# Kernel optimization log

Hardware: AMD Instinct MI355X
Metric: run time of the kernel (lower is better)

## Reference

```python
import jax, jax.numpy as jnp
import numpy as np

L = 2        # n_layers
F = 128      # in_features == out_features (GRUCell + highway constraint)
O = 128
N = 1024     # nodes
B = 8        # batch
D = 3        # edge directions (weight.size(0))


def setup_inputs() -> dict:
    key = jax.random.key(0)
    ks = jax.random.split(key, 10)
    s = 1.0 / np.sqrt(F)
    u = lambda k, shp: jax.random.uniform(k, shp, jnp.float32, minval=-s, maxval=s)
    return {
        "inputs": jax.random.normal(ks[0], (N, B, F), jnp.float32),
        "adj": jax.random.uniform(ks[1], (D, B, N, N), jnp.float32),
        "W": u(ks[2], (L, D, F, O)),            # GCN weight per layer/direction
        "Bc": u(ks[3], (L, D, O)),              # GCN bias
        "Wh": u(ks[4], (L, F, O)),              # highway weight
        "Bh": u(ks[5], (L, O)),                 # highway bias
        "Wih": u(ks[6], (L, 3 * O, O)),         # GRUCell input weights
        "Whh": u(ks[7], (L, 3 * O, O)),         # GRUCell hidden weights
        "bih": u(ks[8], (L, 3 * O)),
        "bhh": u(ks[9], (L, 3 * O)),
    }


def _gru(x, h, wih, whh, bih, bhh):
    # torch.nn.GRUCell semantics; x,h: [..., O]
    gi = x @ wih.T + bih
    gh = h @ whh.T + bhh
    i_r, i_z, i_n = jnp.split(gi, 3, axis=-1)
    h_r, h_z, h_n = jnp.split(gh, 3, axis=-1)
    r = jax.nn.sigmoid(i_r + h_r)
    z = jax.nn.sigmoid(i_z + h_z)
    n = jnp.tanh(i_n + r * h_n)
    return (1.0 - z) * n + z * h


def reference(inputs, adj, W, Bc, Wh, Bh, Wih, Whh, bih, bhh):
    x = inputs  # [N, B, F]; dropout layers are identity at eval
    for l in range(L):
        # support per direction: [D, B, N, O]
        support = jnp.einsum('nbf,dfo->dbno', x, W[l]) + Bc[l][:, None, None, :]
        # adjacency-weighted aggregation: adj[d,b] @ support[d,b]
        agg = jnp.einsum('dbmn,dbno->dbmo', adj, support)
        # GRU update with hidden = current features, per direction, summed over d
        h = jnp.broadcast_to(jnp.transpose(x, (1, 0, 2))[None], agg.shape)
        hnew = _gru(agg, h, Wih[l], Whh[l], bih[l], bhh[l])
        out = jnp.transpose(jnp.sum(hnew, axis=0), (1, 0, 2))  # [N, B, O]
        out = jax.nn.relu(out)  # activation='relu'
        # highway gate (highway='relu')
        t = jax.nn.relu(jnp.einsum('nbf,fo->nbo', x, Wh[l]) + Bh[l])
        x = out * t + x * (1.0 - t)
    return x
```

## Files before the change

kernel.cpp:

```cpp
#include <hip/hip_runtime.h>
#include <math.h>

#define N_NODES 1024
#define BATCH   8
#define FEAT    128
#define NDIR    3
#define NB      (N_NODES*BATCH)
#define G3      384

typedef __bf16 bf16_t;
using bf16x8 = __attribute__((ext_vector_type(8))) __bf16;
using bf16x4 = __attribute__((ext_vector_type(4))) __bf16;
using f32x4  = __attribute__((ext_vector_type(4))) float;

#define GLOAD_LDS16(g, l) \
    __builtin_amdgcn_global_load_lds((const __attribute__((address_space(1))) void*)(g), \
                                     (__attribute__((address_space(3))) void*)(l), 16, 0, 0)

template<int R>
__device__ __forceinline__ void stage_swz(const bf16_t* __restrict__ src, int stride,
                                          int k0, bf16_t* lds, int w, int lane)
{
    #pragma unroll
    for (int q = 0; q < R/32; ++q) {
        int rbase = w*(R/4) + q*8;
        int row = rbase + (lane >> 3);
        int seg = (lane & 7) ^ (row & 7);
        GLOAD_LDS16(src + (size_t)row*stride + k0 + seg*8,
                    (char*)lds + (size_t)rbase*128);
    }
}

__device__ __forceinline__ void stageA_f32(const float* __restrict__ src, int k0,
                                           bf16_t* lds, int w, int lane)
{
    #pragma unroll
    for (int q = 0; q < 2; ++q) {
        int rbase = w*16 + q*8;
        int row = rbase + (lane >> 3);
        int s   = lane & 7;
        int seg = s ^ (row & 7);
        const float* g = src + (size_t)row*1024 + k0 + seg*8;
        float4 v0 = *reinterpret_cast<const float4*>(g);
        float4 v1 = *reinterpret_cast<const float4*>(g + 4);
        bf16x8 pk;
        pk[0]=(bf16_t)(v0.x-0.5f); pk[1]=(bf16_t)(v0.y-0.5f);
        pk[2]=(bf16_t)(v0.z-0.5f); pk[3]=(bf16_t)(v0.w-0.5f);
        pk[4]=(bf16_t)(v1.x-0.5f); pk[5]=(bf16_t)(v1.y-0.5f);
        pk[6]=(bf16_t)(v1.z-0.5f); pk[7]=(bf16_t)(v1.w-0.5f);
        *reinterpret_cast<bf16x8*>(&lds[row*64 + s*8]) = pk;
    }
}

template<int MI, int NJ>
__device__ __forceinline__ void mfma_swz(const bf16_t* As, const bf16_t* Bs,
                                         f32x4 (&acc)[MI][NJ], int wr, int wc, int lane)
{
    #pragma unroll
    for (int ks = 0; ks < 64; ks += 32) {
        int bslot = ks/8 + (lane >> 4);
        int sx = bslot ^ (lane & 7);
        bf16x8 af[MI], bfv[NJ];
        #pragma unroll
        for (int i = 0; i < MI; ++i) {
            int row = wr*MI*16 + i*16 + (lane & 15);
            af[i] = *reinterpret_cast<const bf16x8*>(&As[row*64 + sx*8]);
        }
        #pragma unroll
        for (int j = 0; j < NJ; ++j) {
            int row = wc*NJ*16 + j*16 + (lane & 15);
            bfv[j] = *reinterpret_cast<const bf16x8*>(&Bs[row*64 + sx*8]);
        }
        #pragma unroll
        for (int i = 0; i < MI; ++i) {
            #pragma unroll
            for (int j = 0; j < NJ; ++j)
                acc[i][j] = __builtin_amdgcn_mfma_f32_16x16x32_bf16(af[i], bfv[j], acc[i][j], 0, 0, 0);
        }
    }
}

__device__ __forceinline__ float fast_sigmoid(float x)
{
    float t = __builtin_amdgcn_exp2f(-1.442695041f * x);
    return __builtin_amdgcn_rcpf(1.0f + t);
}
__device__ __forceinline__ float fast_tanh(float x)
{
    float ax = fabsf(x);
    float t = __builtin_amdgcn_exp2f(-2.885390082f * ax);
    float r = (1.0f - t) * __builtin_amdgcn_rcpf(1.0f + t);
    return copysignf(r, x);
}

__global__ __launch_bounds__(128) void k_wprep(
    const float* __restrict__ W, const float* __restrict__ Wh,
    const float* __restrict__ Whh, const float* __restrict__ Wih,
    bf16_t* __restrict__ wsup,
    bf16_t* __restrict__ wihc)
{
    int m = blockIdx.x, l = blockIdx.y, k = threadIdx.x;
    float w;
    bf16_t* dst;
    bool patB = false;
    if (m < 384) {
        int d = m >> 7, o = m & 127;
        w = W[((size_t)(l*3 + d)*128 + k)*128 + o];
        dst = wsup + ((size_t)l*896 + m)*384;
    } else if (m < 512) {
        int o = m - 384;
        w = Wh[((size_t)l*128 + k)*128 + o];
        dst = wsup + ((size_t)l*896 + m)*384;
    } else if (m < 896) {
        int c = m - 512;
        w = Whh[((size_t)l*384 + c)*128 + k];
        dst = wsup + ((size_t)l*896 + m)*384;
    } else {
        int c = m - 896;
        w = Wih[((size_t)l*384 + c)*128 + k];
        dst = wihc + ((size_t)l*384 + c)*384;
        patB = true;
    }
    bf16_t hi = (bf16_t)w;
    bf16_t lo = (bf16_t)(w - (float)hi);
    if (patB) { dst[k] = hi; dst[128 + k] = hi; dst[256 + k] = lo; }
    else      { dst[k] = hi; dst[128 + k] = lo; dst[256 + k] = hi; }
}

__global__ __launch_bounds__(256) void k_xcat(
    const float* __restrict__ X, bf16_t* __restrict__ xcat,
    float* __restrict__ colsum2)
{
    int idx = blockIdx.x * 256 + threadIdx.x;
    if (idx < 2*3072) colsum2[idx] = 0.0f;
    int k = idx & 127, r = idx >> 7;
    int n = r >> 3, b = r & 7;
    float v = X[idx];
    bf16_t hi = (bf16_t)v;
    bf16_t lo = (bf16_t)(v - (float)hi);
    bf16_t* dst = xcat + ((size_t)(b*1024 + n))*384 + k;
    dst[0] = hi; dst[128] = hi; dst[256] = lo;
}

__global__ __launch_bounds__(256, 2) void k_sup2(
    const bf16_t* __restrict__ Wcat,
    const bf16_t* __restrict__ xcat,
    const float* __restrict__ Bcl,
    const float* __restrict__ Bhl,
    const float* __restrict__ bhhl,
    bf16_t* __restrict__ supt,
    float* __restrict__ tbuf,
    bf16_t* __restrict__ ghb,
    float* __restrict__ colsum)
{
    __shared__ bf16_t As[2][128*64];
    __shared__ bf16_t Bs[2][128*64];
    const int t = threadIdx.x, lane = t & 63, w = t >> 6;
    const int wr = w >> 1, wc = w & 1;
    const int n0 = blockIdx.x * 128;
    const int m0 = blockIdx.y * 128;
    const int b  = blockIdx.z;
    const bf16_t* Arow = Wcat + (size_t)m0 * 384;
    const bf16_t* Brow = xcat + ((size_t)b * 1024 + n0) * 384;

    f32x4 acc[4][4] = {};
    stage_swz<128>(Arow, 384, 0, As[0], w, lane);
    stage_swz<128>(Brow, 384, 0, Bs[0], w, lane);
    __syncthreads();
    #pragma unroll
    for (int kt = 0; kt < 6; ++kt) {
        if (kt + 1 < 6) {
            stage_swz<128>(Arow, 384, (kt+1)*64, As[(kt+1)&1], w, lane);
            stage_swz<128>(Brow, 384, (kt+1)*64, Bs[(kt+1)&1], w, lane);
        }
        mfma_swz<4,4>(As[kt&1], Bs[kt&1], acc, wr, wc, lane);
        __syncthreads();
    }
    #pragma unroll
    for (int i = 0; i < 4; ++i) {
        int mb = m0 + wr*64 + i*16 + ((lane >> 4) * 4);
        if (mb < 384) {
            #pragma unroll
            for (int rg = 0; rg < 4; ++rg) {
                int m = mb + rg;
                int d = m >> 7, o = m & 127;
                float bv = Bcl[d*128 + o];
                float psum = 0.0f;
                #pragma unroll
                for (int j = 0; j < 4; ++j) {
                    int n = n0 + wc*64 + j*16 + (lane & 15);
                    bf16_t sv = (bf16_t)(acc[i][j][rg] + bv);
                    supt[((size_t)((d*8 + b)*128 + o))*1024 + n] = sv;
                    psum += (float)sv;
                }
                psum += __shfl_xor(psum, 1, 64);
                psum += __shfl_xor(psum, 2, 64);
                psum += __shfl_xor(psum, 4, 64);
                psum += __shfl_xor(psum, 8, 64);
                if ((lane & 15) == 0)
                    atomicAdd(&colsum[(d*8 + b)*128 + o], psum);
            }
        } else if (mb < 512) {
            #pragma unroll
            for (int j = 0; j < 4; ++j) {
                int n = n0 + wc*64 + j*16 + (lane & 15);
                #pragma unroll
                for (int rg = 0; rg < 4; ++rg) {
                    int o = mb + rg - 384;
                    tbuf[((size_t)(b*128 + o))*1024 + n] =
                        fmaxf(acc[i][j][rg] + Bhl[o], 0.0f);
                }
            }
        } else {
            #pragma unroll
            for (int j = 0; j < 4; ++j) {
                int n = n0 + wc*64 + j*16 + (lane & 15);
                int c = mb - 512;
                bf16x4 pk;
                #pragma unroll
                for (int rg = 0; rg < 4; ++rg)
                    pk[rg] = (bf16_t)(acc[i][j][rg] + bhhl[c + rg]);
                *reinterpret_cast<bf16x4*>(&ghb[((size_t)(b*1024 + n))*384 + c]) = pk;
            }
        }
    }
}

__global__ __launch_bounds__(256, 3) void k_agg(
    const float* __restrict__ adjf,
    const bf16_t* __restrict__ supt,
    const float* __restrict__ colsum,
    bf16_t* __restrict__ aggcat)
{
    __shared__ bf16_t As[2][64*64];
    __shared__ bf16_t Bs[2][128*64];
    const int t = threadIdx.x, lane = t & 63, w = t >> 6;
    const int wr = w >> 1, wc = w & 1;
    const int m0 = blockIdx.x * 64;
    const int z  = blockIdx.y;
    const float*  Af = adjf + (size_t)z * 1024 * 1024 + (size_t)m0 * 1024;
    const bf16_t* Brow = supt + (size_t)z * 128 * 1024;

    f32x4 acc[2][4] = {};
    stageA_f32(Af, 0, As[0], w, lane);
    stage_swz<128>(Brow, 1024, 0, Bs[0], w, lane);
    __syncthreads();
    #pragma unroll
    for (int kt = 0; kt < 16; ++kt) {
        if (kt + 1 < 16) {
            stageA_f32(Af, (kt+1)*64, As[(kt+1)&1], w, lane);
            stage_swz<128>(Brow, 1024, (kt+1)*64, Bs[(kt+1)&1], w, lane);
        }
        mfma_swz<2,4>(As[kt&1], Bs[kt&1], acc, wr, wc, lane);
        __syncthreads();
    }
    #pragma unroll
    for (int i = 0; i < 2; ++i) {
        #pragma unroll
        for (int rg = 0; rg < 4; ++rg) {
            size_t m = (size_t)z*1024 + m0 + wr*32 + i*16 + ((lane >> 4) * 4) + rg;
            bf16_t* row = aggcat + m*384;
            #pragma unroll
            for (int j = 0; j < 4; ++j) {
                int o = wc*64 + j*16 + (lane & 15);
                float v = acc[i][j][rg] + 0.5f * colsum[z*128 + o];
                bf16_t hi = (bf16_t)v;
                bf16_t lo = (bf16_t)(v - (float)hi);
                row[o] = hi; row[128 + o] = lo; row[256 + o] = hi;
            }
        }
    }
}

__global__ __launch_bounds__(256, 2) void k_gi(
    const bf16_t* __restrict__ A,
    const bf16_t* __restrict__ B,
    const float*  __restrict__ bias,
    bf16_t* __restrict__ girz,
    float* __restrict__ gin)
{
    __shared__ bf16_t As[2][128*64];
    __shared__ bf16_t Bs[2][128*64];
    const int t = threadIdx.x, lane = t & 63, w = t >> 6;
    const int wr = w >> 1, wc = w & 1;
    const int m0 = blockIdx.x * 128;
    const int c0 = blockIdx.y * 128;
    const bf16_t* Arow = A + (size_t)m0 * 384;
    const bf16_t* Brow = B + (size_t)c0 * 384;

    f32x4 acc[4][4] = {};
    stage_swz<128>(Arow, 384, 0, As[0], w, lane);
    stage_swz<128>(Brow, 384, 0, Bs[0], w, lane);
    __syncthreads();
    #pragma unroll
    for (int kt = 0; kt < 6; ++kt) {
        if (kt + 1 < 6) {
            stage_swz<128>(Arow, 384, (kt+1)*64, As[(kt+1)&1], w, lane);
            stage_swz<128>(Brow, 384, (kt+1)*64, Bs[(kt+1)&1], w, lane);
        }
        mfma_swz<4,4>(As[kt&1], Bs[kt&1], acc, wr, wc, lane);
        __syncthreads();
    }
    #pragma unroll
    for (int j = 0; j < 4; ++j) {
        int c = c0 + wc*64 + j*16 + (lane & 15);
        float bv = bias[c];
        #pragma unroll
        for (int i = 0; i < 4; ++i) {
            #pragma unroll
            for (int rg = 0; rg < 4; ++rg) {
                int m = m0 + wr*64 + i*16 + ((lane >> 4) * 4) + rg;
                float v = acc[i][j][rg] + bv;
                if (c < 256) girz[(size_t)m*256 + c] = (bf16_t)v;
                else         gin[(size_t)m*128 + (c - 256)] = v;
            }
        }
    }
}

__global__ __launch_bounds__(256) void k_gates(
    const bf16_t* __restrict__ girz, const float* __restrict__ gin,
    const bf16_t* __restrict__ ghb,
    bf16_t* xcat,
    const float* __restrict__ tbuf,
    float* __restrict__ Xout, int write_xcat)
{
    __shared__ float ts[128*17];
    const int b = blockIdx.y, n0 = blockIdx.x * 16;
    const int tid = threadIdx.x;
    {
        int o = tid >> 1, nh = (tid & 1) * 8;
        const float* src = tbuf + ((size_t)(b*128 + o))*1024 + n0 + nh;
        float4 v0 = *reinterpret_cast<const float4*>(src);
        float4 v1 = *reinterpret_cast<const float4*>(src + 4);
        float* dst = &ts[o*17 + nh];
        dst[0]=v0.x; dst[1]=v0.y; dst[2]=v0.z; dst[3]=v0.w;
        dst[4]=v1.x; dst[5]=v1.y; dst[6]=v1.z; dst[7]=v1.w;
    }
    __syncthreads();
    #pragma unroll
    for (int p = 0; p < 8; ++p) {
        int e = p*256 + tid;
        int nn = e >> 7, o = e & 127;
        int n = n0 + nn;
        size_t rb = (size_t)(b*1024 + n);
        bf16_t* xr = xcat + rb*384;
        float h = (float)xr[o] + (float)xr[256 + o];
        const bf16_t* ghr = ghb + rb*G3;
        float g_r = (float)ghr[o], g_z = (float)ghr[128+o], g_n = (float)ghr[256+o];
        float acc = 0.0f;
        #pragma unroll
        for (int d = 0; d < 3; ++d) {
            size_t rr = (size_t)((d*8 + b)*1024 + n);
            float i_r = (float)girz[rr*256 + o];
            float i_z = (float)girz[rr*256 + 128 + o];
            float i_n = gin[rr*128 + o];
            float rg = fast_sigmoid(i_r + g_r);
            float zg = fast_sigmoid(i_z + g_z);
            float ng = fast_tanh(i_n + rg * g_n);
            acc += (1.0f - zg) * ng + zg * h;
        }
        float outv = fmaxf(acc, 0.0f);
        float tg = ts[o*17 + nn];
        float res = outv * tg + h * (1.0f - tg);
        if (Xout) Xout[(size_t)(n*8 + b)*128 + o] = res;
        if (write_xcat) {
            bf16_t hi = (bf16_t)res;
            bf16_t lo = (bf16_t)(res - (float)hi);
            xr[o] = hi; xr[128 + o] = hi; xr[256 + o] = lo;
        }
    }
}

extern "C" void kernel_launch(void* const* d_in, const int* in_sizes, int n_in,
                              void* d_out, int out_size, void* d_ws, size_t ws_size,
                              hipStream_t stream) {
    const float* inputs = (const float*)d_in[0];
    const float* adj    = (const float*)d_in[1];
    const float* W      = (const float*)d_in[2];
    const float* Bc     = (const float*)d_in[3];
    const float* Wh     = (const float*)d_in[4];
    const float* Bh     = (const float*)d_in[5];
    const float* Wih    = (const float*)d_in[6];
    const float* Whh    = (const float*)d_in[7];
    const float* bih    = (const float*)d_in[8];
    const float* bhh    = (const float*)d_in[9];

    char* ws = (char*)d_ws;
    float*  tbuf   = (float*)ws;   ws += (size_t)8*128*1024*4;
    bf16_t* xcat   = (bf16_t*)ws;  ws += (size_t)8*1024*384*2;
    bf16_t* ghb    = (bf16_t*)ws;  ws += (size_t)NB*G3*2;
    bf16_t* supt   = (bf16_t*)ws;  ws += (size_t)24*128*1024*2;
    bf16_t* aggcat = (bf16_t*)ws;  ws += (size_t)3*NB*384*2;
    bf16_t* girz   = (bf16_t*)ws;  ws += (size_t)3*NB*256*2;
    float*  gin    = (float*)ws;   ws += (size_t)3*NB*128*4;
    float*  colsum2= (float*)ws;   ws += (size_t)2*24*128*4;
    bf16_t* wsup   = (bf16_t*)ws;  ws += (size_t)2*896*384*2;
    bf16_t* wihc   = (bf16_t*)ws;

    k_wprep<<<dim3(1280, 2), dim3(128), 0, stream>>>(W, Wh, Whh, Wih, wsup, wihc);
    k_xcat<<<dim3(4096), dim3(256), 0, stream>>>(inputs, xcat, colsum2);

    for (int l = 0; l < 2; ++l) {
        float* colsum = colsum2 + l*3072;
        k_sup2<<<dim3(8, 7, 8), dim3(256), 0, stream>>>(
            wsup + (size_t)l*896*384, xcat, Bc + l*3*128, Bh + l*128, bhh + l*G3,
            supt, tbuf, ghb, colsum);
        k_agg<<<dim3(16, 24), dim3(256), 0, stream>>>(adj, supt, colsum, aggcat);
        k_gi<<<dim3(192, 3), dim3(256), 0, stream>>>(
            aggcat, wihc + (size_t)l*384*384, bih + l*G3, girz, gin);
        k_gates<<<dim3(64, 8), dim3(256), 0, stream>>>(
            girz, gin, ghb, xcat, tbuf,
            (l == 1) ? (float*)d_out : (float*)nullptr, (l == 0) ? 1 : 0);
    }
}
```

Baseline: 316.2 us.

## Fuse adjacency aggregation with GRU input-gate GEMM via LDS-resident tile

Merges k_agg and k_gi into one kernel. The aggregated 64x128 tile, split into bf16 hi/lo parts, now stays in shared memory and is multiplied directly by the Wih weights, which stream through a reused LDS pool. This removes the aggcat global round-trip and one kernel launch. In exchange, each block recomputes the GEMM against the full Wih matrix for only 64 rows, occupancy drops from 3 to 2 blocks per CU, and the 24x16=384-block grid is small.

```diff
diff --git a/kernel.cpp b/kernel.cpp
--- a/kernel.cpp
+++ b/kernel.cpp
@@ -226,93 +226,118 @@
     }
 }
 
-__global__ __launch_bounds__(256, 3) void k_agg(
+__device__ __forceinline__ int aggls_off(int row, int k)
+{
+    return row*256 + (((k >> 3) ^ (row & 15)) << 3) + (k & 7);
+}
+
+__global__ __launch_bounds__(256, 2) void k_aggi(
     const float* __restrict__ adjf,
     const bf16_t* __restrict__ supt,
     const float* __restrict__ colsum,
-    bf16_t* __restrict__ aggcat)
-{
-    __shared__ bf16_t As[2][64*64];
-    __shared__ bf16_t Bs[2][128*64];
+    const bf16_t* __restrict__ wihcL,
+    const float* __restrict__ biasL,
+    bf16_t* __restrict__ girz,
+    float* __restrict__ gin)
+{
+    __shared__ char pool[49152];
+    __shared__ bf16_t aggls[64*256];
+    bf16_t* As  = (bf16_t*)pool;
+    bf16_t* Bs  = (bf16_t*)(pool + 16384);
+    bf16_t* BsG = (bf16_t*)pool;
+
     const int t = threadIdx.x, lane = t & 63, w = t >> 6;
     const int wr = w >> 1, wc = w & 1;
     const int m0 = blockIdx.x * 64;
     const int z  = blockIdx.y;
-    const float*  Af = adjf + (size_t)z * 1024 * 1024 + (size_t)m0 * 1024;
+    const float*  Af   = adjf + (size_t)z * 1024 * 1024 + (size_t)m0 * 1024;
     const bf16_t* Brow = supt + (size_t)z * 128 * 1024;
 
     f32x4 acc[2][4] = {};
-    stageA_f32(Af, 0, As[0], w, lane);
-    stage_swz<128>(Brow, 1024, 0, Bs[0], w, lane);
+    stageA_f32(Af, 0, As, w, lane);
+    stage_swz<128>(Brow, 1024, 0, Bs, w, lane);
     __syncthreads();
     #pragma unroll
     for (int kt = 0; kt < 16; ++kt) {
         if (kt + 1 < 16) {
-            stageA_f32(Af, (kt+1)*64, As[(kt+1)&1], w, lane);
-            stage_swz<128>(Brow, 1024, (kt+1)*64, Bs[(kt+1)&1], w, lane);
-        }
-        mfma_swz<2,4>(As[kt&1], Bs[kt&1], acc, wr, wc, lane);
+            stageA_f32(Af, (kt+1)*64, As + ((kt+1)&1)*4096, w, lane);
+            stage_swz<128>(Brow, 1024, (kt+1)*64, Bs + ((kt+1)&1)*8192, w, lane);
+        }
+        mfma_swz<2,4>(As + (kt&1)*4096, Bs + (kt&1)*8192, acc, wr, wc, lane);
         __syncthreads();
     }
+
+    stage_swz<128>(wihcL, 384, 0, BsG, w, lane);
+
     #pragma unroll
     for (int i = 0; i < 2; ++i) {
         #pragma unroll
         for (int rg = 0; rg < 4; ++rg) {
-            size_t m = (size_t)z*1024 + m0 + wr*32 + i*16 + ((lane >> 4) * 4) + rg;
-            bf16_t* row = aggcat + m*384;
+            int row = wr*32 + i*16 + ((lane >> 4) * 4) + rg;
             #pragma unroll
             for (int j = 0; j < 4; ++j) {
                 int o = wc*64 + j*16 + (lane & 15);
                 float v = acc[i][j][rg] + 0.5f * colsum[z*128 + o];
                 bf16_t hi = (bf16_t)v;
                 bf16_t lo = (bf16_t)(v - (float)hi);
-                row[o] = hi; row[128 + o] = lo; row[256 + o] = hi;
-            }
-        }
-    }
-}
-
-__global__ __launch_bounds__(256, 2) void k_gi(
-    const bf16_t* __restrict__ A,
-    const bf16_t* __restrict__ B,
-    const float*  __restrict__ bias,
-    bf16_t* __restrict__ girz,
-    float* __restrict__ gin)
-{
-    __shared__ bf16_t As[2][128*64];
-    __shared__ bf16_t Bs[2][128*64];
-    const int t = threadIdx.x, lane = t & 63, w = t >> 6;
-    const int wr = w >> 1, wc = w & 1;
-    const int m0 = blockIdx.x * 128;
-    const int c0 = blockIdx.y * 128;
-    const bf16_t* Arow = A + (size_t)m0 * 384;
-    const bf16_t* Brow = B + (size_t)c0 * 384;
-
-    f32x4 acc[4][4] = {};
-    stage_swz<128>(Arow, 384, 0, As[0], w, lane);
-    stage_swz<128>(Brow, 384, 0, Bs[0], w, lane);
+                aggls[aggls_off(row, o)]       = hi;
+                aggls[aggls_off(row, 128 + o)] = lo;
+            }
+        }
+    }
     __syncthreads();
-    #pragma unroll
-    for (int kt = 0; kt < 6; ++kt) {
-        if (kt + 1 < 6) {
-            stage_swz<128>(Arow, 384, (kt+1)*64, As[(kt+1)&1], w, lane);
-            stage_swz<128>(Brow, 384, (kt+1)*64, Bs[(kt+1)&1], w, lane);
-        }
-        mfma_swz<4,4>(As[kt&1], Bs[kt&1], acc, wr, wc, lane);
-        __syncthreads();
-    }
-    #pragma unroll
-    for (int j = 0; j < 4; ++j) {
-        int c = c0 + wc*64 + j*16 + (lane & 15);
-        float bv = bias[c];
-        #pragma unroll
-        for (int i = 0; i < 4; ++i) {
-            #pragma unroll
-            for (int rg = 0; rg < 4; ++rg) {
-                int m = m0 + wr*64 + i*16 + ((lane >> 4) * 4) + rg;
-                float v = acc[i][j][rg] + bv;
-                if (c < 256) girz[(size_t)m*256 + c] = (bf16_t)v;
-                else         gin[(size_t)m*128 + (c - 256)] = v;
+
+    #pragma unroll
+    for (int cc = 0; cc < 3; ++cc) {
+        f32x4 a2[2][4] = {};
+        #pragma unroll
+        for (int kt = 0; kt < 6; ++kt) {
+            int it = cc*6 + kt;
+            if (it + 1 < 18) {
+                int nc = (it+1)/6, nk = (it+1)%6;
+                stage_swz<128>(wihcL + (size_t)nc*128*384, 384, nk*64,
+                               BsG + ((it+1)&1)*8192, w, lane);
+            }
+            const bf16_t* Bcur = BsG + (it&1)*8192;
+            int akk = (kt < 4 ? kt : kt - 4) * 64;
+            #pragma unroll
+            for (int ks = 0; ks < 64; ks += 32) {
+                bf16x8 af[2], bfv[4];
+                #pragma unroll
+                for (int i = 0; i < 2; ++i) {
+                    int row = wr*32 + i*16 + (lane & 15);
+                    int ss = ((akk + ks)/8 + (lane >> 4)) ^ (lane & 15);
+                    af[i] = *reinterpret_cast<const bf16x8*>(&aggls[row*256 + ss*8]);
+                }
+                #pragma unroll
+                for (int j = 0; j < 4; ++j) {
+                    int row = wc*64 + j*16 + (lane & 15);
+                    int sx = (ks/8 + (lane >> 4)) ^ (lane & 7);
+                    bfv[j] = *reinterpret_cast<const bf16x8*>(&Bcur[row*64 + sx*8]);
+                }
+                #pragma unroll
+                for (int i = 0; i < 2; ++i) {
+                    #pragma unroll
+                    for (int j = 0; j < 4; ++j)
+                        a2[i][j] = __builtin_amdgcn_mfma_f32_16x16x32_bf16(af[i], bfv[j], a2[i][j], 0, 0, 0);
+                }
+            }
+            __syncthreads();
+        }
+        #pragma unroll
+        for (int j = 0; j < 4; ++j) {
+            int c = cc*128 + wc*64 + j*16 + (lane & 15);
+            float bv = biasL[c];
+            #pragma unroll
+            for (int i = 0; i < 2; ++i) {
+                #pragma unroll
+                for (int rg = 0; rg < 4; ++rg) {
+                    int rloc = wr*32 + i*16 + ((lane >> 4) * 4) + rg;
+                    size_t m = (size_t)z*1024 + m0 + rloc;
+                    float v = a2[i][j][rg] + bv;
+                    if (c < 256) girz[m*256 + c] = (bf16_t)v;
+                    else         gin[m*128 + (c - 256)] = v;
+                }
             }
         }
     }
@@ -391,7 +416,6 @@
     bf16_t* xcat   = (bf16_t*)ws;  ws += (size_t)8*1024*384*2;
     bf16_t* ghb    = (bf16_t*)ws;  ws += (size_t)NB*G3*2;
     bf16_t* supt   = (bf16_t*)ws;  ws += (size_t)24*128*1024*2;
-    bf16_t* aggcat = (bf16_t*)ws;  ws += (size_t)3*NB*384*2;
     bf16_t* girz   = (bf16_t*)ws;  ws += (size_t)3*NB*256*2;
     float*  gin    = (float*)ws;   ws += (size_t)3*NB*128*4;
     float*  colsum2= (float*)ws;   ws += (size_t)2*24*128*4;
@@ -406,9 +430,8 @@
         k_sup2<<<dim3(8, 7, 8), dim3(256), 0, stream>>>(
             wsup + (size_t)l*896*384, xcat, Bc + l*3*128, Bh + l*128, bhh + l*G3,
             supt, tbuf, ghb, colsum);
-        k_agg<<<dim3(16, 24), dim3(256), 0, stream>>>(adj, supt, colsum, aggcat);
-        k_gi<<<dim3(192, 3), dim3(256), 0, stream>>>(
-            aggcat, wihc + (size_t)l*384*384, bih + l*G3, girz, gin);
+        k_aggi<<<dim3(16, 24), dim3(256), 0, stream>>>(
+            adj, supt, colsum, wihc + (size_t)l*384*384, bih + l*G3, girz, gin);
         k_gates<<<dim3(64, 8), dim3(256), 0, stream>>>(
             girz, gin, ghb, xcat, tbuf,
             (l == 1) ? (float*)d_out : (float*)nullptr, (l == 0) ? 1 : 0);
```

Measured after the change: 294.5 us. 6.9% less time.
